# Performance work log

Hardware: AMD Instinct MI355X
Metric: run time of the kernel (lower is better)

## Reference

```python
import jax, jax.numpy as jnp
import numpy as np

N_IMG = 512
N_ANGLES = 180


def _bilinear(img, sy, sx):
    """Bilinear sample img at float coords (sy, sx); zero outside the image."""
    n = img.shape[0]
    y0 = jnp.floor(sy)
    x0 = jnp.floor(sx)
    wy = sy - y0
    wx = sx - x0
    y0i = y0.astype(jnp.int32)
    x0i = x0.astype(jnp.int32)

    def gather(yi, xi):
        valid = (yi >= 0) & (yi < n) & (xi >= 0) & (xi < n)
        yc = jnp.clip(yi, 0, n - 1)
        xc = jnp.clip(xi, 0, n - 1)
        return jnp.where(valid, img[yc, xc], jnp.zeros((), img.dtype))

    v00 = gather(y0i, x0i)
    v01 = gather(y0i, x0i + 1)
    v10 = gather(y0i + 1, x0i)
    v11 = gather(y0i + 1, x0i + 1)
    return (v00 * (1 - wy) * (1 - wx) + v01 * (1 - wy) * wx
            + v10 * wy * (1 - wx) + v11 * wy * wx)


def _radon(img, angles):
    """skimage-style radon: rotate image by each angle, sum along axis 0.
    Returns sinogram of shape (n_detectors, n_angles) = (N, len(angles))."""
    n = img.shape[0]
    c = (n - 1) * 0.5  # rotation about image center
    coords = jnp.arange(n, dtype=img.dtype) - c
    yc, xc = jnp.meshgrid(coords, coords, indexing="ij")  # (N, N)

    def one_angle(theta_deg):
        t = jnp.deg2rad(theta_deg.astype(img.dtype))
        co, si = jnp.cos(t), jnp.sin(t)
        # inverse-rotation sampling coordinates (CCW rotation of the image)
        sx = co * xc + si * yc + c
        sy = -si * xc + co * yc + c
        rotated = _bilinear(img, sy, sx)  # (N, N)
        return rotated.sum(axis=0)        # projection along detector rows -> (N,)

    sino = jax.vmap(one_angle)(angles)  # (n_angles, N)
    return sino.T                        # (N, n_angles)


def setup_inputs() -> dict:
    key = jax.random.key(0)
    img = jax.random.uniform(key, (N_IMG, N_IMG), dtype=jnp.float32)  # nonnegative PET activity
    angles = jnp.arange(N_ANGLES, dtype=jnp.int32)  # degrees 0..179 (skimage default)
    return {"img": img, "angles": angles}


def reference(img, angles):
    return _radon(img, angles)
```

## Files before the change

### kernel.cpp

```cpp
#include <hip/hip_runtime.h>
#include <hip/hip_fp16.h>
#include <stdint.h>

#define N 512
#define NA 180
#define TD 64
#define TI 64
#define TW 96
#define TILE_DW (36 * 256)
#define PP 708
#define PR 704
#define POFF 96

#define WS_IMGPB  0
#define WS_IMGTPB (PR * PP)
#define WS_TAB    (2 * PR * PP)
#define WS_FLAGS  (WS_TAB + 4 * NA)
#define WS_OUTT   997888

typedef _Float16 hh2 __attribute__((ext_vector_type(2)));
union H2U { uint32_t u; hh2 h; };

__device__ __forceinline__ hh2 cvt_pkrtz(float a, float b) {
    return __builtin_bit_cast(hh2, __builtin_amdgcn_cvt_pkrtz(a, b));
}

__device__ __forceinline__ void load16_to_lds(const uint32_t* g, uint32_t* l) {
    __builtin_amdgcn_global_load_lds(
        (const __attribute__((address_space(1))) void*)g,
        (__attribute__((address_space(3))) void*)l,
        16 , 0 , 0 );
}

__global__ __launch_bounds__(256) void pad_kernel(const float* __restrict__ img,
                                                  const int* __restrict__ angles,
                                                  uint32_t* __restrict__ imgPB,
                                                  uint32_t* __restrict__ imgTPB,
                                                  float4* __restrict__ tab,
                                                  int* __restrict__ flags,
                                                  float* __restrict__ outT) {
    __shared__ float lds[65 * 66];
    const int lane = threadIdx.x & 63;
    const int wq   = threadIdx.x >> 6;
    const int bx = blockIdx.x, by = blockIdx.y;
    const int b  = by * 11 + bx;

    if (b < 90) {
        float4 z; z.x = z.y = z.z = z.w = 0.0f;
        ((float4*)outT)[b * 256 + threadIdx.x] = z;
    }
    if (b == 120 && threadIdx.x < NA) {
        float t = (float)angles[threadIdx.x] * 0.017453292519943295f;
        float si = sinf(t), co = cosf(t);
        int useT = fabsf(si) > fabsf(co);
        float4 e;
        if (useT) { e.x = co; e.y = -si; e.z = si; e.w = co; }
        else      { e.x = si; e.y = co;  e.z = co; e.w = -si; }
        tab[threadIdx.x] = e;
        flags[threadIdx.x] = useT;
    }

    for (int idx = threadIdx.x; idx < 65 * 65; idx += 256) {
        int r = idx / 65, cc = idx - r * 65;
        int y = by * 64 + r - POFF, x = bx * 64 + cc - POFF;
        bool in = ((unsigned)y < N) && ((unsigned)x < N);
        lds[r * 66 + cc] = in ? img[y * N + x] : 0.0f;
    }
    __syncthreads();
#pragma unroll
    for (int j = 0; j < 16; ++j) {
        int r = wq * 16 + j;
        float v0 = lds[r * 66 + lane], v1 = lds[r * 66 + lane + 1];
        __half2 h = __halves2half2(__float2half(v0), __float2half(v1));
        imgPB[(size_t)(by * 64 + r) * PP + bx * 64 + lane] = *(uint32_t*)&h;
        float t0 = lds[lane * 66 + r], t1 = lds[(lane + 1) * 66 + r];
        __half2 ht = __halves2half2(__float2half(t0), __float2half(t1));
        imgTPB[(size_t)(bx * 64 + r) * PP + by * 64 + lane] = *(uint32_t*)&ht;
    }
}

__global__ __launch_bounds__(512, 8) void radon_kernel(const uint32_t* __restrict__ imgPB,
                                                       const uint32_t* __restrict__ imgTPB,
                                                       const float4* __restrict__ tab,
                                                       const int* __restrict__ flags,
                                                       float* __restrict__ outT) {
    __shared__ uint32_t tile[TILE_DW];

    const int tid  = threadIdx.x;
    const int lane = tid & 63;
    const int wave = tid >> 6;
    const int d0 = blockIdx.x * TD;
    const int a  = blockIdx.y;
    const int i0 = blockIdx.z * TI;

    const float c = 255.5f;
    const float4 tb = tab[a];
    const float au = tb.x, bus = tb.y, av = tb.z, bvs = tb.w;

    const float fi0 = (float)i0 - c, fi1 = (float)(i0 + TI - 1) - c;
    const float xc0 = (float)d0 - c, xc1 = (float)(d0 + TD - 1) - c;
    const float buA = fmaf(bus, xc0, c), buB = fmaf(bus, xc1, c);
    const float bvA = fmaf(bvs, xc0, c), bvB = fmaf(bvs, xc1, c);
    const float buMin = fminf(buA, buB), buMax = fmaxf(buA, buB);
    const float bvMin = fminf(bvA, bvB), bvMax = fmaxf(bvA, bvB);
    const float fiLoU = (au >= 0.0f) ? fi0 : fi1, fiHiU = (au >= 0.0f) ? fi1 : fi0;
    const float fiLoV = (av >= 0.0f) ? fi0 : fi1, fiHiV = (av >= 0.0f) ? fi1 : fi0;
    const float umin = fmaf(au, fiLoU, buMin), umax = fmaf(au, fiHiU, buMax);
    const float vmin = fmaf(av, fiLoV, bvMin), vmax = fmaf(av, fiHiV, bvMax);

    if (umin > (float)N || umax < -1.0f || vmin > (float)N || vmax < -1.0f) return;

    const int ub0 = (((int)floorf(umin)) - 1) & ~3;
    const int vb  = ((int)floorf(vmin)) - 1;

    const uint32_t* __restrict__ src = flags[a] ? imgTPB : imgPB;
    const uint32_t* gbase = src + (vb + POFF) * PP + (ub0 + POFF);

#pragma unroll
    for (int s = 0; s < 5; ++s) {
        int chunk = s * 8 + wave;
        if (chunk < 36) {
            int tt = chunk * 256 + (lane << 2);
            int r  = tt / TW;
            int cc = tt - r * TW;
            load16_to_lds(gbase + r * PP + cc, &tile[chunk * 256]);
        }
    }
    __syncthreads();

    const float xcl = (float)(d0 + lane) - c;
    const float buL = fmaf(bus, xcl, c) - (float)ub0;
    const float bvL = fmaf(bvs, xcl, c) - (float)vb;

    float s = 0.0f;
    float fi = (float)(i0 + wave * 8) - c;
#pragma unroll
    for (int k = 0; k < 8; ++k) {
        float u = fmaf(au, fi, buL);
        float v = fmaf(av, fi, bvL);
        fi += 1.0f;
        float wx = __builtin_amdgcn_fractf(u);
        float wy = __builtin_amdgcn_fractf(v);
        int iu = (int)u, iv = (int)v;
        int ai = iv * TW + iu;
        H2U P0, P1;
        P0.u = tile[ai];
        P1.u = tile[ai + TW];
        hh2 wy2 = cvt_pkrtz(wy, wy);
        hh2 m   = wy2 * (P1.h - P0.h) + P0.h;
        hh2 wv  = cvt_pkrtz(1.0f - wx, wx);
#if __has_builtin(__builtin_amdgcn_fdot2)
        s = __builtin_amdgcn_fdot2(wv, m, s, false);
#else
        s += (1.0f - wx) * (float)m.x + wx * (float)m.y;
#endif
    }

    __syncthreads();
    float* ft = (float*)tile;
    ft[tid] = s;
    __syncthreads();
    if (tid < 64) {
        float r = ft[tid]       + ft[tid + 64]  + ft[tid + 128] + ft[tid + 192]
                + ft[tid + 256] + ft[tid + 320] + ft[tid + 384] + ft[tid + 448];
        atomicAdd(&outT[a * 512 + d0 + tid], r);
    }
}

__global__ __launch_bounds__(256) void txo_kernel(const float* __restrict__ outT,
                                                  float* __restrict__ out) {
    __shared__ float lds[64 * 65];
    const int lane = threadIdx.x & 63;
    const int wq   = threadIdx.x >> 6;
    const int d0 = blockIdx.x * 64;
    const int a0 = blockIdx.y * 64;
#pragma unroll
    for (int j = 0; j < 16; ++j) {
        int r = wq * 16 + j;
        int a = a0 + r;
        lds[r * 65 + lane] = (a < NA) ? outT[a * 512 + d0 + lane] : 0.0f;
    }
    __syncthreads();
#pragma unroll
    for (int j = 0; j < 16; ++j) {
        int r = wq * 16 + j;
        int aa = a0 + lane;
        if (aa < NA) out[(d0 + r) * NA + aa] = lds[lane * 65 + r];
    }
}

extern "C" void kernel_launch(void* const* d_in, const int* in_sizes, int n_in,
                              void* d_out, int out_size, void* d_ws, size_t ws_size,
                              hipStream_t stream) {
    const float* img  = (const float*)d_in[0];
    const int* angles = (const int*)d_in[1];
    float* out = (float*)d_out;
    float* ws  = (float*)d_ws;

    uint32_t* imgPB  = (uint32_t*)(ws + WS_IMGPB);
    uint32_t* imgTPB = (uint32_t*)(ws + WS_IMGTPB);
    float4*   tab    = (float4*)(ws + WS_TAB);
    int*      flags  = (int*)(ws + WS_FLAGS);
    float*    outT   = ws + WS_OUTT;

    dim3 pgrid(11, 11);
    pad_kernel<<<pgrid, 256, 0, stream>>>(img, angles, imgPB, imgTPB, tab, flags, outT);

    dim3 grid(N / TD, NA, N / TI);
    radon_kernel<<<grid, 512, 0, stream>>>(imgPB, imgTPB, tab, flags, outT);

    dim3 tgrid(512 / 64, 3);
    txo_kernel<<<tgrid, 256, 0, stream>>>(outT, out);
}
```

Before: 100.6 us.

## Process two row phases per radon block to halve block count and atomics

Each radon block now covers 128 rows in two sequential 64-row phases, reloading the LDS tile per phase and accumulating into one register sum. This halves the grid size and the number of atomicAdds and reductions per output, at the cost of serialising the tile load and compute within a block with no overlap. The pad kernel moves to 512 threads per block, and the inner loop steps u/v incrementally instead of recomputing from fi. Sampling coordinates change from one fmaf per row to repeated additions, so float rounding in u and v can differ slightly.

```diff
diff --git a/kernel.cpp b/kernel.cpp
--- a/kernel.cpp
+++ b/kernel.cpp
@@ -5,7 +5,7 @@
 #define N 512
 #define NA 180
 #define TD 64
-#define TI 64
+#define TI 128
 #define TW 96
 #define TILE_DW (36 * 256)
 #define PP 708
@@ -32,7 +32,7 @@
         16 , 0 , 0 );
 }
 
-__global__ __launch_bounds__(256) void pad_kernel(const float* __restrict__ img,
+__global__ __launch_bounds__(512) void pad_kernel(const float* __restrict__ img,
                                                   const int* __restrict__ angles,
                                                   uint32_t* __restrict__ imgPB,
                                                   uint32_t* __restrict__ imgTPB,
@@ -40,27 +40,28 @@
                                                   int* __restrict__ flags,
                                                   float* __restrict__ outT) {
     __shared__ float lds[65 * 66];
-    const int lane = threadIdx.x & 63;
-    const int wq   = threadIdx.x >> 6;
+    const int tid  = threadIdx.x;
+    const int lane = tid & 63;
+    const int wq   = tid >> 6;
     const int bx = blockIdx.x, by = blockIdx.y;
     const int b  = by * 11 + bx;
 
-    if (b < 90) {
+    if (b < 45) {
         float4 z; z.x = z.y = z.z = z.w = 0.0f;
-        ((float4*)outT)[b * 256 + threadIdx.x] = z;
-    }
-    if (b == 120 && threadIdx.x < NA) {
-        float t = (float)angles[threadIdx.x] * 0.017453292519943295f;
+        ((float4*)outT)[b * 512 + tid] = z;
+    }
+    if (b == 120 && tid < NA) {
+        float t = (float)angles[tid] * 0.017453292519943295f;
         float si = sinf(t), co = cosf(t);
         int useT = fabsf(si) > fabsf(co);
         float4 e;
         if (useT) { e.x = co; e.y = -si; e.z = si; e.w = co; }
         else      { e.x = si; e.y = co;  e.z = co; e.w = -si; }
-        tab[threadIdx.x] = e;
-        flags[threadIdx.x] = useT;
-    }
-
-    for (int idx = threadIdx.x; idx < 65 * 65; idx += 256) {
+        tab[tid] = e;
+        flags[tid] = useT;
+    }
+
+    for (int idx = tid; idx < 65 * 65; idx += 512) {
         int r = idx / 65, cc = idx - r * 65;
         int y = by * 64 + r - POFF, x = bx * 64 + cc - POFF;
         bool in = ((unsigned)y < N) && ((unsigned)x < N);
@@ -68,8 +69,8 @@
     }
     __syncthreads();
 #pragma unroll
-    for (int j = 0; j < 16; ++j) {
-        int r = wq * 16 + j;
+    for (int j = 0; j < 8; ++j) {
+        int r = wq * 8 + j;
         float v0 = lds[r * 66 + lane], v1 = lds[r * 66 + lane + 1];
         __half2 h = __halves2half2(__float2half(v0), __float2half(v1));
         imgPB[(size_t)(by * 64 + r) * PP + bx * 64 + lane] = *(uint32_t*)&h;
@@ -97,63 +98,85 @@
     const float4 tb = tab[a];
     const float au = tb.x, bus = tb.y, av = tb.z, bvs = tb.w;
 
-    const float fi0 = (float)i0 - c, fi1 = (float)(i0 + TI - 1) - c;
     const float xc0 = (float)d0 - c, xc1 = (float)(d0 + TD - 1) - c;
     const float buA = fmaf(bus, xc0, c), buB = fmaf(bus, xc1, c);
     const float bvA = fmaf(bvs, xc0, c), bvB = fmaf(bvs, xc1, c);
     const float buMin = fminf(buA, buB), buMax = fmaxf(buA, buB);
     const float bvMin = fminf(bvA, bvB), bvMax = fmaxf(bvA, bvB);
-    const float fiLoU = (au >= 0.0f) ? fi0 : fi1, fiHiU = (au >= 0.0f) ? fi1 : fi0;
-    const float fiLoV = (av >= 0.0f) ? fi0 : fi1, fiHiV = (av >= 0.0f) ? fi1 : fi0;
-    const float umin = fmaf(au, fiLoU, buMin), umax = fmaf(au, fiHiU, buMax);
-    const float vmin = fmaf(av, fiLoV, bvMin), vmax = fmaf(av, fiHiV, bvMax);
-
-    if (umin > (float)N || umax < -1.0f || vmin > (float)N || vmax < -1.0f) return;
-
-    const int ub0 = (((int)floorf(umin)) - 1) & ~3;
-    const int vb  = ((int)floorf(vmin)) - 1;
+
+    {
+        const float fi0 = (float)i0 - c, fi1 = (float)(i0 + TI - 1) - c;
+        const float fiLoU = (au >= 0.0f) ? fi0 : fi1, fiHiU = (au >= 0.0f) ? fi1 : fi0;
+        const float fiLoV = (av >= 0.0f) ? fi0 : fi1, fiHiV = (av >= 0.0f) ? fi1 : fi0;
+        if (fmaf(au, fiLoU, buMin) > (float)N || fmaf(au, fiHiU, buMax) < -1.0f ||
+            fmaf(av, fiLoV, bvMin) > (float)N || fmaf(av, fiHiV, bvMax) < -1.0f)
+            return;
+    }
 
     const uint32_t* __restrict__ src = flags[a] ? imgTPB : imgPB;
-    const uint32_t* gbase = src + (vb + POFF) * PP + (ub0 + POFF);
-
-#pragma unroll
-    for (int s = 0; s < 5; ++s) {
-        int chunk = s * 8 + wave;
-        if (chunk < 36) {
-            int tt = chunk * 256 + (lane << 2);
-            int r  = tt / TW;
-            int cc = tt - r * TW;
-            load16_to_lds(gbase + r * PP + cc, &tile[chunk * 256]);
+
+    const float xcl = (float)(d0 + lane) - c;
+    const float buLb = fmaf(bus, xcl, c);
+    const float bvLb = fmaf(bvs, xcl, c);
+
+    const int t0g  = wave * 256 + (lane << 2);
+    const int q0   = t0g / TW;
+    const int c0   = t0g - q0 * TW;
+    const int goff0 = q0 * PP + c0;
+
+    float s = 0.0f;
+#pragma unroll
+    for (int ph = 0; ph < 2; ++ph) {
+        const int ip = i0 + ph * 64;
+        const float fi0 = (float)ip - c, fi1 = (float)(ip + 63) - c;
+        const float fiLoU = (au >= 0.0f) ? fi0 : fi1, fiHiU = (au >= 0.0f) ? fi1 : fi0;
+        const float fiLoV = (av >= 0.0f) ? fi0 : fi1, fiHiV = (av >= 0.0f) ? fi1 : fi0;
+        const float umin = fmaf(au, fiLoU, buMin), umax = fmaf(au, fiHiU, buMax);
+        const float vmin = fmaf(av, fiLoV, bvMin), vmax = fmaf(av, fiHiV, bvMax);
+        const bool live = !(umin > (float)N || umax < -1.0f ||
+                            vmin > (float)N || vmax < -1.0f);
+
+        const int ub0 = (((int)floorf(umin)) - 1) & ~3;
+        const int vb  = ((int)floorf(vmin)) - 1;
+
+        __syncthreads();
+        if (live) {
+            const uint32_t* gb = src + (vb + POFF) * PP + (ub0 + POFF) + goff0;
+            int cc = c0;
+#pragma unroll
+            for (int st = 0; st < 5; ++st) {
+                int chunk = st * 8 + wave;
+                if (chunk < 36) load16_to_lds(gb, &tile[chunk * 256]);
+                cc += 32;
+                int wrap = (cc >= TW);
+                cc = wrap ? cc - TW : cc;
+                gb += 21 * PP + 32 + (wrap ? (PP - TW) : 0);
+            }
         }
-    }
-    __syncthreads();
-
-    const float xcl = (float)(d0 + lane) - c;
-    const float buL = fmaf(bus, xcl, c) - (float)ub0;
-    const float bvL = fmaf(bvs, xcl, c) - (float)vb;
-
-    float s = 0.0f;
-    float fi = (float)(i0 + wave * 8) - c;
-#pragma unroll
-    for (int k = 0; k < 8; ++k) {
-        float u = fmaf(au, fi, buL);
-        float v = fmaf(av, fi, bvL);
-        fi += 1.0f;
-        float wx = __builtin_amdgcn_fractf(u);
-        float wy = __builtin_amdgcn_fractf(v);
-        int iu = (int)u, iv = (int)v;
-        int ai = iv * TW + iu;
-        H2U P0, P1;
-        P0.u = tile[ai];
-        P1.u = tile[ai + TW];
-        hh2 wy2 = cvt_pkrtz(wy, wy);
-        hh2 m   = wy2 * (P1.h - P0.h) + P0.h;
-        hh2 wv  = cvt_pkrtz(1.0f - wx, wx);
-#if __has_builtin(__builtin_amdgcn_fdot2)
-        s = __builtin_amdgcn_fdot2(wv, m, s, false);
-#else
-        s += (1.0f - wx) * (float)m.x + wx * (float)m.y;
-#endif
+        __syncthreads();
+        if (live) {
+            const float buL = buLb - (float)ub0;
+            const float bvL = bvLb - (float)vb;
+            const float fiw = (float)(ip + wave * 8) - c;
+            float u = fmaf(au, fiw, buL);
+            float v = fmaf(av, fiw, bvL);
+#pragma unroll
+            for (int k = 0; k < 8; ++k) {
+                float wx = __builtin_amdgcn_fractf(u);
+                float wy = __builtin_amdgcn_fractf(v);
+                int iu = (int)u, iv = (int)v;
+                int ai = iv * TW + iu;
+                H2U P0, P1;
+                P0.u = tile[ai];
+                P1.u = tile[ai + TW];
+                hh2 wy2 = cvt_pkrtz(wy, wy);
+                hh2 m   = wy2 * (P1.h - P0.h) + P0.h;
+                hh2 wv  = cvt_pkrtz(1.0f - wx, wx);
+                s = __builtin_amdgcn_fdot2(wv, m, s, false);
+                u += au;
+                v += av;
+            }
+        }
     }
 
     __syncthreads();
@@ -204,7 +227,7 @@
     float*    outT   = ws + WS_OUTT;
 
     dim3 pgrid(11, 11);
-    pad_kernel<<<pgrid, 256, 0, stream>>>(img, angles, imgPB, imgTPB, tab, flags, outT);
+    pad_kernel<<<pgrid, 512, 0, stream>>>(img, angles, imgPB, imgTPB, tab, flags, outT);
 
     dim3 grid(N / TD, NA, N / TI);
     radon_kernel<<<grid, 512, 0, stream>>>(imgPB, imgTPB, tab, flags, outT);
```

Measured after the change: 97.33 us. 1.03x faster.
